# Performance work log

Measured on AMD Instinct MI355X. Metric: run time of the kernel, lower is better.

Reference implementation:

```python
import jax, jax.numpy as jnp
import numpy as np


def _scan_dir(x, A, B, reverse):
    """First-order linear recurrence h_i = A*h_{i-1} + B*x_i along last axis (W).
    x: [Bsz, C, H, W]; A, B: [C]. reverse=True scans right-to-left but returns
    states in original index order (matching torch scan_backward)."""
    xs = jnp.moveaxis(x, -1, 0)  # [W, Bsz, C, H]
    Ab = A[None, :, None]
    Bb = B[None, :, None]
    def step(h, xi):
        h = Ab * h + Bb * xi
        return h, h
    h0 = jnp.zeros_like(xs[0])
    _, hs = jax.lax.scan(step, h0, xs, reverse=reverse)
    return jnp.moveaxis(hs, 0, -1)  # [Bsz, C, H, W]


def _conv1x1(x, W, b):
    # x: [B,Cin,H,W], W: [Cout,Cin], b: [Cout]
    return jnp.einsum('bchw,dc->bdhw', x, W) + b[None, :, None, None]


def setup_inputs() -> dict:
    key = jax.random.key(0)
    ks = jax.random.split(key, 10)
    B, C, H, W = 8, 64, 128, 128
    D = 128  # hidden_dim
    return {
        'F_in': jax.random.normal(ks[0], (B, C, H, W), dtype=jnp.float32),
        'prior': jax.random.uniform(ks[1], (B, 1, H, W), dtype=jnp.float32),
        'Wi': jax.random.normal(ks[2], (D, C), dtype=jnp.float32) * 0.05,
        'bi': jnp.zeros((D,), dtype=jnp.float32),
        'A_param': jax.random.normal(ks[3], (D,), dtype=jnp.float32),
        'B_param': jax.random.normal(ks[4], (D,), dtype=jnp.float32),
        'alpha': jnp.float32(0.1),
        'gamma': jnp.float32(0.1),
        'Wf': jax.random.normal(ks[5], (D, 4 * D), dtype=jnp.float32) * 0.05,
        'bf': jnp.zeros((D,), dtype=jnp.float32),
        'Wo': jax.random.normal(ks[6], (C, D), dtype=jnp.float32) * 0.05,
        'bo': jnp.zeros((C,), dtype=jnp.float32),
    }


def reference(F_in, prior, Wi, bi, A_param, B_param, alpha, gamma, Wf, bf, Wo, bo):
    # prior has 1 channel, repeated to C channels (prior already matches HxW)
    prior_r = jnp.broadcast_to(prior, F_in.shape)
    F_mod = F_in + alpha * prior_r
    x = _conv1x1(F_mod, Wi, bi)  # [B, D, H, W]
    A = jnp.tanh(A_param)
    Bp = B_param
    h_lr = _scan_dir(x, A, Bp, reverse=False)
    h_rl = _scan_dir(x, A, Bp, reverse=True)
    xt = jnp.swapaxes(x, 2, 3)  # scan over H axis
    h_tb = jnp.swapaxes(_scan_dir(xt, A, Bp, reverse=False), 2, 3)
    h_bt = jnp.swapaxes(_scan_dir(xt, A, Bp, reverse=True), 2, 3)
    h = jnp.concatenate([h_lr, h_rl, h_tb, h_bt], axis=1)  # [B, 4D, H, W]
    h = _conv1x1(h, Wf, bf)   # fusion -> [B, D, H, W]
    out = _conv1x1(h, Wo, bo)  # output_proj -> [B, C, H, W]
    return F_mod + gamma * out
```

## Files before the change

### kernel.cpp

```cpp
#include <hip/hip_runtime.h>
#include <hip/hip_bf16.h>

typedef unsigned int u32;
typedef unsigned short u16;
typedef float f32x2 __attribute__((ext_vector_type(2)));
typedef float f32x4 __attribute__((ext_vector_type(4)));
using bf16x8 = __attribute__((ext_vector_type(8))) short;
using f32x4v = __attribute__((ext_vector_type(4))) float;

#define DEVINL __device__ __forceinline__

constexpr int XLDS = 16384;
constexpr int SCAN_LDS = 32768;
constexpr int XS = 132;
constexpr int LDS_X = 128 * XS * 2;

DEVINL float bf2f(u16 u) { union { u32 i; float f; } v; v.i = ((u32)u) << 16; return v.f; }
DEVINL float bf2f_lo(u32 u) { union { u32 i; float f; } v; v.i = u << 16; return v.f; }
DEVINL float bf2f_hi(u32 u) { union { u32 i; float f; } v; v.i = u & 0xffff0000u; return v.f; }
DEVINL u16 f2bf(float f) {
  __hip_bfloat16 h = __float2bfloat16(f);
  u16 r; __builtin_memcpy(&r, &h, 2); return r;
}
DEVINL u32 pack2(float a, float b) { return (u32)f2bf(a) | ((u32)f2bf(b) << 16); }

__global__ __launch_bounds__(256) void k_pre(
    const float* __restrict__ Wf, const float* __restrict__ Wo,
    const float* __restrict__ bf_, const float* __restrict__ bo,
    const float* __restrict__ A_param, const float* __restrict__ Wi,
    float* __restrict__ A_t, float* __restrict__ beff,
    u16* __restrict__ Mrow, u16* __restrict__ Wi_bf) {
  const int wg = blockIdx.x, t = threadIdx.x;
  if (wg < 128) {
    const int idx = wg * 256 + t;
    const int cout = idx >> 9;
    const int k = idx & 511;
    float s = 0.f;
    for (int d = 0; d < 128; ++d) s = fmaf(Wo[cout * 128 + d], Wf[d * 512 + k], s);
    const int dir = k >> 7, dm = k & 127;
    Mrow[(dir * 64 + cout) * 128 + dm] = f2bf(s);
  } else if (wg == 128) {
    if (t < 128) A_t[t] = tanhf(A_param[t]);
    if (t < 64) {
      float s = bo[t];
      for (int d = 0; d < 128; ++d) s = fmaf(Wo[t * 128 + d], bf_[d], s);
      beff[t] = s;
    }
  } else {
#pragma unroll
    for (int k = 0; k < 32; ++k) {
      const int i = t + k * 256;
      Wi_bf[i] = f2bf(Wi[i]);
    }
  }
}

extern __shared__ char smem[];

__global__ __launch_bounds__(256, 4) void k_x(
    const float* __restrict__ F_in, const float* __restrict__ prior,
    const u16* __restrict__ Wi_bf, const float* __restrict__ bi,
    const float* __restrict__ alpha_p, u16* __restrict__ x2) {
  char* FT = smem;

  const int t = threadIdx.x;
  const int lane = t & 63, wv = t >> 6, l15 = lane & 15, kg = lane >> 4;
  const int bid = blockIdx.x, b = bid >> 7, h = bid & 127;

  {
    const int w = t & 127, ch = t >> 7;
    const float alpha = alpha_p[0];
    const float pv = prior[(b * 128 + h) * 128 + w];
    const float* Fb = F_in + ((size_t)b * 64 + ch * 32) * 16384 + h * 128 + w;
    const u32 sw = (u32)((w & 7) << 4);
    char* rowp = FT + w * 128;
#pragma unroll
    for (int q = 0; q < 4; ++q) {
      float fv[8];
#pragma unroll
      for (int j = 0; j < 8; ++j) fv[j] = fmaf(alpha, pv, Fb[(q * 8 + j) * 16384]);
      uint4 pk;
      pk.x = pack2(fv[0], fv[1]); pk.y = pack2(fv[2], fv[3]);
      pk.z = pack2(fv[4], fv[5]); pk.w = pack2(fv[6], fv[7]);
      *(uint4*)(rowp + ((u32)(ch * 64 + q * 16) ^ sw)) = pk;
    }
  }
  __syncthreads();

  bf16x8 bF[2][2];
#pragma unroll
  for (int wj = 0; wj < 2; ++wj)
#pragma unroll
    for (int ks = 0; ks < 2; ++ks) {
      const int row = wv * 32 + wj * 16 + l15;
      bF[wj][ks] = *(const bf16x8*)(FT + row * 128 + ((u32)(ks * 64 + kg * 16) ^ ((u32)((row & 7) << 4))));
    }

  {
    f32x4v acc[8][2];
#pragma unroll
    for (int dt = 0; dt < 8; ++dt) {
      const f32x4 bv = *(const f32x4*)(bi + dt * 16 + kg * 4);
      const f32x4v bvv = { bv.x, bv.y, bv.z, bv.w };
#pragma unroll
      for (int wj = 0; wj < 2; ++wj) acc[dt][wj] = bvv;
    }
#pragma unroll
    for (int ks = 0; ks < 2; ++ks)
#pragma unroll
      for (int dt = 0; dt < 8; ++dt) {
        const bf16x8 aWi = *(const bf16x8*)(Wi_bf + (dt * 16 + l15) * 64 + ks * 32 + kg * 8);
        acc[dt][0] = __builtin_amdgcn_mfma_f32_16x16x32_bf16(aWi, bF[0][ks], acc[dt][0], 0, 0, 0);
        acc[dt][1] = __builtin_amdgcn_mfma_f32_16x16x32_bf16(aWi, bF[1][ks], acc[dt][1], 0, 0, 0);
      }
    u16* xg = x2 + (size_t)(b * 128 + h) * 16384;
#pragma unroll
    for (int dt = 0; dt < 8; ++dt)
#pragma unroll
      for (int wj = 0; wj < 2; ++wj) {
        const int w = wv * 32 + wj * 16 + l15;
        const int dl = dt * 16 + kg * 4;
        uint2 pk;
        pk.x = pack2(acc[dt][wj][0], acc[dt][wj][1]);
        pk.y = pack2(acc[dt][wj][2], acc[dt][wj][3]);
        *(uint2*)(xg + w * 128 + dl) = pk;
      }
  }
}

template <bool REV>
DEVINL void scan_local(char* buf, int dp, int chunk, f32x2 A2, f32x2 B2) {
  f32x2 h = { 0.f, 0.f };
  const u32 cb = (u32)(dp * 4);
  const int s = chunk * 32;
  u32 nx[8];
#pragma unroll
  for (int j = 0; j < 8; ++j) {
    const int i = REV ? (127 - (s + j)) : (s + j);
    nx[j] = *(const u32*)(buf + i * 128 + (cb ^ ((u32)((i & 7) << 4))));
  }
  for (int ib = 0; ib < 32; ib += 8) {
    u32 cur[8];
#pragma unroll
    for (int j = 0; j < 8; ++j) cur[j] = nx[j];
    if (ib + 8 < 32) {
#pragma unroll
      for (int j = 0; j < 8; ++j) {
        const int i2 = s + ib + 8 + j;
        const int i = REV ? (127 - i2) : i2;
        nx[j] = *(const u32*)(buf + i * 128 + (cb ^ ((u32)((i & 7) << 4))));
      }
    }
#pragma unroll
    for (int j = 0; j < 8; ++j) {
      const int i2 = s + ib + j;
      const int i = REV ? (127 - i2) : i2;
      const f32x2 xv = { bf2f_lo(cur[j]), bf2f_hi(cur[j]) };
      h = A2 * h + B2 * xv;
      *(u32*)(buf + i * 128 + (cb ^ ((u32)((i & 7) << 4)))) = pack2(h.x, h.y);
    }
  }
}

template <bool REV>
DEVINL void scan_fix(char* buf, int dp, int chunk, f32x2 A2) {
  if (chunk == 0) return;
  f32x2 q = A2;
#pragma unroll
  for (int k = 0; k < 5; ++k) q *= q;
  const u32 cb = (u32)(dp * 4);
  f32x2 C = { 0.f, 0.f };
  for (int k = 0; k < chunk; ++k) {
    const int i2 = k * 32 + 31;
    const int i = REV ? (127 - i2) : i2;
    const u32 v = *(const u32*)(buf + i * 128 + (cb ^ ((u32)((i & 7) << 4))));
    const f32x2 xv = { bf2f_lo(v), bf2f_hi(v) };
    C = C * q + xv;
  }
  f32x2 p = A2;
  const int s = chunk * 32;
  u32 nx[8];
#pragma unroll
  for (int j = 0; j < 8; ++j) {
    const int i = REV ? (127 - (s + j)) : (s + j);
    nx[j] = *(const u32*)(buf + i * 128 + (cb ^ ((u32)((i & 7) << 4))));
  }
  for (int ib = 0; ib < 32; ib += 8) {
    u32 cur[8];
#pragma unroll
    for (int j = 0; j < 8; ++j) cur[j] = nx[j];
    if (ib + 8 < 32) {
#pragma unroll
      for (int j = 0; j < 8; ++j) {
        const int i2 = s + ib + 8 + j;
        const int i = REV ? (127 - i2) : i2;
        nx[j] = *(const u32*)(buf + i * 128 + (cb ^ ((u32)((i & 7) << 4))));
      }
    }
#pragma unroll
    for (int j = 0; j < 8; ++j) {
      const int i2 = s + ib + j;
      const int i = REV ? (127 - i2) : i2;
      const f32x2 xv = { bf2f_lo(cur[j]), bf2f_hi(cur[j]) };
      const f32x2 hv = p * C + xv;
      *(u32*)(buf + i * 128 + (cb ^ ((u32)((i & 7) << 4)))) = pack2(hv.x, hv.y);
      p *= A2;
    }
  }
}

DEVINL void run_scans(char* bufA, char* bufB, int t, int e,
                      const float* __restrict__ A_t, const float* __restrict__ Bp) {
  const int dp = t & 31, chunk = (t >> 5) & 3, dir = t >> 7;
  const int dgp = e * 64 + dp * 2;
  const f32x2 a = *(const f32x2*)(A_t + dgp);
  const f32x2 bb = *(const f32x2*)(Bp + dgp);
  char* sb = dir ? bufB : bufA;
  if (dir == 0) scan_local<false>(sb, dp, chunk, a, bb);
  else          scan_local<true >(sb, dp, chunk, a, bb);
  __syncthreads();
  if (dir == 0) scan_fix<false>(sb, dp, chunk, a);
  else          scan_fix<true >(sb, dp, chunk, a);
}

DEVINL void combine64(const char* buf, const u16* __restrict__ Mrow, int dir, int e,
                      int lane, int wv, f32x4v (&acc2)[4][2]) {
  const int l15 = lane & 15, kg = lane >> 4;
#pragma unroll
  for (int ks = 0; ks < 2; ++ks) {
    bf16x8 afr[4], bfr[2];
#pragma unroll
    for (int ct = 0; ct < 4; ++ct)
      afr[ct] = *(const bf16x8*)(Mrow + ((size_t)dir * 64 + ct * 16 + l15) * 128 + e * 64 + ks * 32 + kg * 8);
#pragma unroll
    for (int pt = 0; pt < 2; ++pt) {
      const int row = wv * 32 + pt * 16 + l15;
      bfr[pt] = *(const bf16x8*)(buf + row * 128 + ((u32)(ks * 64 + kg * 16) ^ ((u32)((row & 7) << 4))));
    }
#pragma unroll
    for (int ct = 0; ct < 4; ++ct)
#pragma unroll
      for (int pt = 0; pt < 2; ++pt)
        acc2[ct][pt] = __builtin_amdgcn_mfma_f32_16x16x32_bf16(bfr[pt], afr[ct], acc2[ct][pt], 0, 0, 0);
  }
}

DEVINL void acc_to_outs(const f32x4v (&acc2)[4][2], int lane, int wv, char* buf) {
  const int l15 = lane & 15, kg = lane >> 4;
#pragma unroll
  for (int ct = 0; ct < 4; ++ct)
#pragma unroll
    for (int pt = 0; pt < 2; ++pt) {
      const int c = ct * 16 + l15;
      const int pos = wv * 32 + pt * 16 + kg * 4;
      *(f32x4v*)(buf + c * 512 + ((u32)(pos * 4) ^ ((u32)((c & 7) << 4)))) = acc2[ct][pt];
    }
}

DEVINL void outs_to_global(const char* buf, u16* __restrict__ og, int t) {
#pragma unroll
  for (int j = 0; j < 16; ++j) {
    const int i = t + j * 256;
    const int c = i >> 6, p2 = (i & 63) * 2;
    const f32x2 v = *(const f32x2*)(buf + c * 512 + ((u32)(p2 * 4) ^ ((u32)((c & 7) << 4))));
    *(u32*)(og + c * 128 + p2) = pack2(v.x, v.y);
  }
}

__global__ __launch_bounds__(256, 5) void k_scan(
    const u16* __restrict__ x2, const float* __restrict__ Bp,
    const float* __restrict__ A_t, const u16* __restrict__ Mrow,
    u16* __restrict__ Shp, u16* __restrict__ Svp) {
  char* bufA = smem;
  char* bufB = smem + 16384;
  const int t = threadIdx.x;
  const int lane = t & 63, wv = t >> 6;
  const int bid = blockIdx.x;
  const int vert = bid & 1;
  const int bid2 = bid >> 1;
  const int b = bid2 >> 8, p = (bid2 >> 1) & 127, e = bid2 & 1;

#pragma unroll
  for (int j = 0; j < 4; ++j) {
    const int idx = t + j * 256;
    const int row = idx >> 3, q = idx & 7;
    const u16* src = vert
        ? x2 + (size_t)(b * 128 + row) * 16384 + p * 128 + e * 64 + q * 8
        : x2 + (size_t)(b * 128 + p) * 16384 + row * 128 + e * 64 + q * 8;
    const uint4 v = *(const uint4*)src;
    const u32 col = (u32)(q * 16) ^ ((u32)((row & 7) << 4));
    *(uint4*)(bufA + row * 128 + col) = v;
    *(uint4*)(bufB + row * 128 + col) = v;
  }
  __syncthreads();

  run_scans(bufA, bufB, t, e, A_t, Bp);
  __syncthreads();

  f32x4v acc2[4][2];
#pragma unroll
  for (int i = 0; i < 4; ++i)
#pragma unroll
    for (int j = 0; j < 2; ++j) acc2[i][j] = (f32x4v)0.f;
  combine64(bufA, Mrow, vert ? 2 : 0, e, lane, wv, acc2);
  combine64(bufB, Mrow, vert ? 3 : 1, e, lane, wv, acc2);
  __syncthreads();

  acc_to_outs(acc2, lane, wv, smem);
  __syncthreads();

  u16* og = (vert ? Svp : Shp) + (size_t)bid2 * 8192;
  outs_to_global(smem, og, t);
}

__global__ __launch_bounds__(256) void k_final(
    const float* __restrict__ F_in, const float* __restrict__ prior,
    const float* __restrict__ alpha_p, const float* __restrict__ gamma_p,
    const float* __restrict__ beff, const u16* __restrict__ Svp,
    const u16* __restrict__ Shp, float* __restrict__ out) {
  u16* Xu = (u16*)smem;
  const int t = threadIdx.x;
  const int bid = blockIdx.x, b = bid >> 6, c = bid & 63;
  const size_t base = (size_t)bid * 16384;

  for (int i = t; i < 2048; i += 256) {
    const int w = i >> 4, q = i & 15;
    const u16* s0 = Svp + ((size_t)((b * 128 + w) * 2)) * 8192 + c * 128 + q * 8;
    const uint4 a4 = *(const uint4*)(s0);
    const uint4 b4 = *(const uint4*)(s0 + 8192);
    const u16* ap = (const u16*)&a4;
    const u16* bp = (const u16*)&b4;
    u32* dst = (u32*)(Xu + w * 132 + q * 8);
#pragma unroll
    for (int k = 0; k < 4; ++k) {
      const float lo = bf2f(ap[k * 2]) + bf2f(bp[k * 2]);
      const float hi = bf2f(ap[k * 2 + 1]) + bf2f(bp[k * 2 + 1]);
      dst[k] = pack2(lo, hi);
    }
  }
  __syncthreads();
  const float alpha = alpha_p[0], gamma = gamma_p[0];
  const float be = beff[c];
  for (int i = t; i < 2048; i += 256) {
    const int hh = i >> 4, w8 = (i & 15) * 8;
    const size_t off = base + hh * 128 + w8;
    const u16* sh0 = Shp + ((size_t)((b * 128 + hh) * 2)) * 8192 + c * 128 + w8;
    const uint4 g0 = *(const uint4*)(sh0);
    const uint4 g1 = *(const uint4*)(sh0 + 8192);
    const u16* p0 = (const u16*)&g0;
    const u16* p1 = (const u16*)&g1;
    const float* Fp = F_in + off;
    float* Op = out + off;
    const float* Pp = prior + (b * 128 + hh) * 128 + w8;
#pragma unroll
    for (int q = 0; q < 8; ++q) {
      const float sv = bf2f(Xu[(w8 + q) * 132 + hh]);
      Op[q] = Fp[q] + alpha * Pp[q] + gamma * (bf2f(p0[q]) + bf2f(p1[q]) + sv + be);
    }
  }
}

extern "C" void kernel_launch(void* const* d_in, const int* in_sizes, int n_in,
                              void* d_out, int out_size, void* d_ws, size_t ws_size,
                              hipStream_t stream) {
  const float* F_in   = (const float*)d_in[0];
  const float* prior  = (const float*)d_in[1];
  const float* Wi     = (const float*)d_in[2];
  const float* bi     = (const float*)d_in[3];
  const float* A_par  = (const float*)d_in[4];
  const float* B_par  = (const float*)d_in[5];
  const float* alpha  = (const float*)d_in[6];
  const float* gamma  = (const float*)d_in[7];
  const float* Wf     = (const float*)d_in[8];
  const float* bf_    = (const float*)d_in[9];
  const float* Wo     = (const float*)d_in[10];
  const float* bo     = (const float*)d_in[11];
  float* out = (float*)d_out;

  char* ws = (char*)d_ws;
  float* A_t   = (float*)ws;
  float* beff  = (float*)(ws + 512);
  u16*   Mrow  = (u16*)(ws + 1024);
  u16*   Wi_bf = (u16*)(ws + 66560);
  u16*   x2    = (u16*)(ws + 82944);
  u16*   Shp   = (u16*)(ws + 82944 + 33554432);
  u16*   Svp   = (u16*)(ws + 82944 + 67108864);

  hipFuncSetAttribute((const void*)k_x,    hipFuncAttributeMaxDynamicSharedMemorySize, XLDS);
  hipFuncSetAttribute((const void*)k_scan, hipFuncAttributeMaxDynamicSharedMemorySize, SCAN_LDS);

  k_pre  <<<130, 256, 0, stream>>>(Wf, Wo, bf_, bo, A_par, Wi, A_t, beff, Mrow, Wi_bf);
  k_x    <<<1024, 256, XLDS, stream>>>(F_in, prior, Wi_bf, bi, alpha, x2);
  k_scan <<<4096, 256, SCAN_LDS, stream>>>(x2, B_par, A_t, Mrow, Shp, Svp);
  k_final<<<512, 256, LDS_X, stream>>>(F_in, prior, alpha, gamma, beff, Svp, Shp, out);
}
```

Measured before the change: 103.8 us.

## Fold B scaling into x projection and use single-pass serial scans

```diff
diff --git a/kernel.cpp b/kernel.cpp
--- a/kernel.cpp
+++ b/kernel.cpp
@@ -60,7 +60,8 @@
 __global__ __launch_bounds__(256, 4) void k_x(
     const float* __restrict__ F_in, const float* __restrict__ prior,
     const u16* __restrict__ Wi_bf, const float* __restrict__ bi,
-    const float* __restrict__ alpha_p, u16* __restrict__ x2) {
+    const float* __restrict__ Bp, const float* __restrict__ alpha_p,
+    u16* __restrict__ x2) {
   char* FT = smem;
 
   const int t = threadIdx.x;
@@ -115,112 +116,63 @@
       }
     u16* xg = x2 + (size_t)(b * 128 + h) * 16384;
 #pragma unroll
-    for (int dt = 0; dt < 8; ++dt)
+    for (int dt = 0; dt < 8; ++dt) {
+      const f32x4 B4 = *(const f32x4*)(Bp + dt * 16 + kg * 4);
+      const f32x4v B4v = { B4.x, B4.y, B4.z, B4.w };
 #pragma unroll
       for (int wj = 0; wj < 2; ++wj) {
+        const f32x4v sv = acc[dt][wj] * B4v;
         const int w = wv * 32 + wj * 16 + l15;
         const int dl = dt * 16 + kg * 4;
         uint2 pk;
-        pk.x = pack2(acc[dt][wj][0], acc[dt][wj][1]);
-        pk.y = pack2(acc[dt][wj][2], acc[dt][wj][3]);
+        pk.x = pack2(sv[0], sv[1]);
+        pk.y = pack2(sv[2], sv[3]);
         *(uint2*)(xg + w * 128 + dl) = pk;
       }
+    }
   }
 }
 
 template <bool REV>
-DEVINL void scan_local(char* buf, int dp, int chunk, f32x2 A2, f32x2 B2) {
+DEVINL void scan_serial(char* buf, int dp, f32x2 A2) {
   f32x2 h = { 0.f, 0.f };
   const u32 cb = (u32)(dp * 4);
-  const int s = chunk * 32;
   u32 nx[8];
 #pragma unroll
   for (int j = 0; j < 8; ++j) {
-    const int i = REV ? (127 - (s + j)) : (s + j);
+    const int i = REV ? (127 - j) : j;
     nx[j] = *(const u32*)(buf + i * 128 + (cb ^ ((u32)((i & 7) << 4))));
   }
-  for (int ib = 0; ib < 32; ib += 8) {
+  for (int ib = 0; ib < 128; ib += 8) {
     u32 cur[8];
 #pragma unroll
     for (int j = 0; j < 8; ++j) cur[j] = nx[j];
-    if (ib + 8 < 32) {
+    if (ib + 8 < 128) {
 #pragma unroll
       for (int j = 0; j < 8; ++j) {
-        const int i2 = s + ib + 8 + j;
+        const int i2 = ib + 8 + j;
         const int i = REV ? (127 - i2) : i2;
         nx[j] = *(const u32*)(buf + i * 128 + (cb ^ ((u32)((i & 7) << 4))));
       }
     }
 #pragma unroll
     for (int j = 0; j < 8; ++j) {
-      const int i2 = s + ib + j;
+      const int i2 = ib + j;
       const int i = REV ? (127 - i2) : i2;
       const f32x2 xv = { bf2f_lo(cur[j]), bf2f_hi(cur[j]) };
-      h = A2 * h + B2 * xv;
+      h = A2 * h + xv;
       *(u32*)(buf + i * 128 + (cb ^ ((u32)((i & 7) << 4)))) = pack2(h.x, h.y);
     }
   }
 }
 
-template <bool REV>
-DEVINL void scan_fix(char* buf, int dp, int chunk, f32x2 A2) {
-  if (chunk == 0) return;
-  f32x2 q = A2;
-#pragma unroll
-  for (int k = 0; k < 5; ++k) q *= q;
-  const u32 cb = (u32)(dp * 4);
-  f32x2 C = { 0.f, 0.f };
-  for (int k = 0; k < chunk; ++k) {
-    const int i2 = k * 32 + 31;
-    const int i = REV ? (127 - i2) : i2;
-    const u32 v = *(const u32*)(buf + i * 128 + (cb ^ ((u32)((i & 7) << 4))));
-    const f32x2 xv = { bf2f_lo(v), bf2f_hi(v) };
-    C = C * q + xv;
-  }
-  f32x2 p = A2;
-  const int s = chunk * 32;
-  u32 nx[8];
-#pragma unroll
-  for (int j = 0; j < 8; ++j) {
-    const int i = REV ? (127 - (s + j)) : (s + j);
-    nx[j] = *(const u32*)(buf + i * 128 + (cb ^ ((u32)((i & 7) << 4))));
-  }
-  for (int ib = 0; ib < 32; ib += 8) {
-    u32 cur[8];
-#pragma unroll
-    for (int j = 0; j < 8; ++j) cur[j] = nx[j];
-    if (ib + 8 < 32) {
-#pragma unroll
-      for (int j = 0; j < 8; ++j) {
-        const int i2 = s + ib + 8 + j;
-        const int i = REV ? (127 - i2) : i2;
-        nx[j] = *(const u32*)(buf + i * 128 + (cb ^ ((u32)((i & 7) << 4))));
-      }
-    }
-#pragma unroll
-    for (int j = 0; j < 8; ++j) {
-      const int i2 = s + ib + j;
-      const int i = REV ? (127 - i2) : i2;
-      const f32x2 xv = { bf2f_lo(cur[j]), bf2f_hi(cur[j]) };
-      const f32x2 hv = p * C + xv;
-      *(u32*)(buf + i * 128 + (cb ^ ((u32)((i & 7) << 4)))) = pack2(hv.x, hv.y);
-      p *= A2;
-    }
-  }
-}
-
-DEVINL void run_scans(char* bufA, char* bufB, int t, int e,
-                      const float* __restrict__ A_t, const float* __restrict__ Bp) {
-  const int dp = t & 31, chunk = (t >> 5) & 3, dir = t >> 7;
-  const int dgp = e * 64 + dp * 2;
-  const f32x2 a = *(const f32x2*)(A_t + dgp);
-  const f32x2 bb = *(const f32x2*)(Bp + dgp);
-  char* sb = dir ? bufB : bufA;
-  if (dir == 0) scan_local<false>(sb, dp, chunk, a, bb);
-  else          scan_local<true >(sb, dp, chunk, a, bb);
-  __syncthreads();
-  if (dir == 0) scan_fix<false>(sb, dp, chunk, a);
-  else          scan_fix<true >(sb, dp, chunk, a);
+DEVINL void run_scans(char* bufA, char* bufB, int t, int e, const float* __restrict__ A_t) {
+  if (t < 64) {
+    const int dp = t & 31, dir = t >> 5;
+    const f32x2 a = *(const f32x2*)(A_t + e * 64 + dp * 2);
+    if (dir == 0) scan_serial<false>(bufA, dp, a);
+    else          scan_serial<true >(bufB, dp, a);
+  }
 }
 
 DEVINL void combine64(const char* buf, const u16* __restrict__ Mrow, int dir, int e,
@@ -268,7 +220,7 @@
 }
 
 __global__ __launch_bounds__(256, 5) void k_scan(
-    const u16* __restrict__ x2, const float* __restrict__ Bp,
+    const u16* __restrict__ x2,
     const float* __restrict__ A_t, const u16* __restrict__ Mrow,
     u16* __restrict__ Shp, u16* __restrict__ Svp) {
   char* bufA = smem;
@@ -294,7 +246,7 @@
   }
   __syncthreads();
 
-  run_scans(bufA, bufB, t, e, A_t, Bp);
+  run_scans(bufA, bufB, t, e, A_t);
   __syncthreads();
 
   f32x4v acc2[4][2];
@@ -390,7 +342,7 @@
   hipFuncSetAttribute((const void*)k_scan, hipFuncAttributeMaxDynamicSharedMemorySize, SCAN_LDS);
 
   k_pre  <<<130, 256, 0, stream>>>(Wf, Wo, bf_, bo, A_par, Wi, A_t, beff, Mrow, Wi_bf);
-  k_x    <<<1024, 256, XLDS, stream>>>(F_in, prior, Wi_bf, bi, alpha, x2);
-  k_scan <<<4096, 256, SCAN_LDS, stream>>>(x2, B_par, A_t, Mrow, Shp, Svp);
+  k_x    <<<1024, 256, XLDS, stream>>>(F_in, prior, Wi_bf, bi, B_par, alpha, x2);
+  k_scan <<<4096, 256, SCAN_LDS, stream>>>(x2, A_t, Mrow, Shp, Svp);
   k_final<<<512, 256, LDS_X, stream>>>(F_in, prior, alpha, gamma, beff, Svp, Shp, out);
 }
```

Measured after the change: 129.5 us. 24.7% more time.
